# Kernel optimization log

Hardware: AMD Instinct MI355X
Metric: run time of the kernel (lower is better)

Reference implementation:

```python
import jax, jax.numpy as jnp
import numpy as np

B, T, V, E, H, S, C, VF, A, L = 32, 32, 32000, 512, 512, 512, 256, 512, 256, 50


def setup_inputs() -> dict:
    key = jax.random.key(0)
    ks = jax.random.split(key, 17)
    sc = lambda k, shp, fan: (jax.random.normal(k, shp, jnp.float32) / np.sqrt(fan)).astype(jnp.float32)
    inp = {
        "tgt": jax.random.randint(ks[0], (B, T), 0, V, dtype=jnp.int64),
        "decoder_state": jax.random.normal(ks[1], (B, H), jnp.float32),
        "category": jax.random.normal(ks[2], (B, C), jnp.float32),
        "v_feature": jax.random.normal(ks[3], (B, VF), jnp.float32),
        "session_outputs": jax.random.normal(ks[4], (B, L, S), jnp.float32),
        "session_mask": jnp.ones((B, L), dtype=bool),
        # learned parameters
        "emb": sc(ks[5], (V, E), E),
        "attn_Wh": sc(ks[6], (H, A), H),
        "attn_Ws": sc(ks[7], (S, A), S),
        "attn_b": jnp.zeros((A,), jnp.float32),
        "attn_v": sc(ks[8], (A,), A),
        "W_ih": sc(ks[9], (3 * H, E + S + C + VF), H),
        "W_hh": sc(ks[10], (3 * H, H), H),
        "b_ih": jnp.zeros((3 * H,), jnp.float32),
        "b_hh": jnp.zeros((3 * H,), jnp.float32),
        "W_out": 0.1 * jax.random.normal(ks[11], (V, H), jnp.float32),  # init.normal_(0, 0.1)
        "b_out": jnp.zeros((V,), jnp.float32),
    }
    return inp


def reference(tgt, decoder_state, category, v_feature, session_outputs, session_mask,
              emb, attn_Wh, attn_Ws, attn_b, attn_v, W_ih, W_hh, b_ih, b_hh, W_out, b_out):
    neg = jnp.finfo(session_outputs.dtype).min
    x = jnp.swapaxes(emb[tgt], 0, 1)                       # T,B,E
    sess_proj = jnp.einsum('bls,sa->bla', session_outputs, attn_Ws) + attn_b  # precompute key proj

    def step(h, x_t):
        # additive (Bahdanau) session attention on last-layer state h: B,H
        q = (h @ attn_Wh)[:, None, :]                      # B,1,A
        e = jnp.einsum('bla,a->bl', jnp.tanh(q + sess_proj), attn_v)
        e = jnp.where(session_mask, e, neg)
        a = jax.nn.softmax(e, axis=-1)                     # B,L
        ctx = jnp.einsum('bl,blh->bh', a, session_outputs)
        inp = jnp.concatenate([x_t, ctx, category, v_feature], axis=-1)
        # single-step GRU (PyTorch gate order: reset, update, new)
        gx = inp @ W_ih.T + b_ih
        gh = h @ W_hh.T + b_hh
        xr, xz, xn = jnp.split(gx, 3, axis=-1)
        hr, hz, hn = jnp.split(gh, 3, axis=-1)
        r = jax.nn.sigmoid(xr + hr)
        z = jax.nn.sigmoid(xz + hz)
        n = jnp.tanh(xn + r * hn)
        h2 = (1.0 - z) * n + z * h
        vocab = h2 @ W_out.T + b_out
        return h2, (vocab, h2)

    _, (vocab_outputs, outputs) = jax.lax.scan(step, decoder_state, x)
    return jnp.swapaxes(vocab_outputs, 0, 1), jnp.swapaxes(outputs, 0, 1)
```

## Files before the change

kernel.cpp:

```cpp
#include <hip/hip_runtime.h>

typedef unsigned short u16;
typedef unsigned int u32;
typedef __attribute__((ext_vector_type(8))) short short8;
typedef __attribute__((ext_vector_type(4))) float f32x4;

#define NB 32
#define NT 32
#define NV 32000
#define NE 512
#define NH 512
#define NS 512
#define NC 256
#define NVF 512
#define NA 256
#define NL 50
#define G3 1536
#define NWB 1792

__device__ __forceinline__ float bf2f(u16 u) {
  union { u32 i; float f; } v; v.i = ((u32)u) << 16; return v.f;
}
__device__ __forceinline__ u16 f2bf(float f) {
  union { float f; u32 i; } v; v.f = f;
  u32 x = v.i;
  return (u16)((x + 0x7fffu + ((x >> 16) & 1u)) >> 16);
}
__device__ __forceinline__ float sigmoidf_(float x) { return 1.f / (1.f + __expf(-x)); }
__device__ __forceinline__ float tanhf_(float x) {
  x = fminf(fmaxf(x, -15.f), 15.f);
  float e = __expf(2.f * x);
  return (e - 1.f) / (e + 1.f);
}
__device__ __forceinline__ void cvt8(u16* dst, const float* src) {
  f32x4 a = *(const f32x4*)src;
  f32x4 b = *(const f32x4*)(src + 4);
  short8 o;
  o[0] = (short)f2bf(a[0]); o[1] = (short)f2bf(a[1]);
  o[2] = (short)f2bf(a[2]); o[3] = (short)f2bf(a[3]);
  o[4] = (short)f2bf(b[0]); o[5] = (short)f2bf(b[1]);
  o[6] = (short)f2bf(b[2]); o[7] = (short)f2bf(b[3]);
  *(short8*)dst = o;
}

__global__ __launch_bounds__(256) void prep_kernel(
    const int* __restrict__ tgt, const float* __restrict__ dec,
    const float* __restrict__ cat, const float* __restrict__ vfe,
    const float* __restrict__ sess, const float* __restrict__ emb,
    const float* __restrict__ Wh, const float* __restrict__ Ws,
    const float* __restrict__ Wih, const float* __restrict__ Whh,
    const float* __restrict__ Wout,
    u16* __restrict__ WB, u16* __restrict__ Wx, u16* __restrict__ Wc,
    u16* __restrict__ X, u16* __restrict__ Ah, float* __restrict__ h_ws,
    u16* __restrict__ Wob, u16* __restrict__ Wst, u16* __restrict__ sessb,
    u16* __restrict__ cvb, u16* __restrict__ Wcv)
{
  int blk = blockIdx.x, tid = threadIdx.x;
  if (blk < 448) {
    int base = (blk * 256 + tid) * 8, j = base >> 9, c = base & 511;
    if (j < G3) cvt8(WB + base, Whh + (size_t)j * 512 + c);
    else {
      int a = j - G3;
      short8 o;
      #pragma unroll
      for (int i = 0; i < 8; i++) o[i] = (short)f2bf(Wh[(size_t)(c + i) * NA + a]);
      *(short8*)(WB + base) = o;
    }
  } else if (blk < 832) {
    int base = ((blk - 448) * 256 + tid) * 8, j = base >> 9, c = base & 511;
    cvt8(Wx + base, Wih + (size_t)j * 1792 + c);
  } else if (blk < 1216) {
    int base = ((blk - 832) * 256 + tid) * 8, j = base >> 9, c = base & 511;
    cvt8(Wc + base, Wih + (size_t)j * 1792 + 512 + c);
  } else if (blk < 1472) {
    int base = ((blk - 1216) * 256 + tid) * 8, tb = base >> 9, e = base & 511;
    cvt8(X + base, emb + (size_t)tgt[tb] * NE + e);
  } else if (blk < 1480) {
    int base = ((blk - 1472) * 256 + tid) * 8;
    cvt8(Ah + base, dec + base);
  } else if (blk < 1488) {
    int base = ((blk - 1480) * 256 + tid) * 8;
    *(f32x4*)(h_ws + base) = *(const f32x4*)(dec + base);
    *(f32x4*)(h_ws + base + 4) = *(const f32x4*)(dec + base + 4);
  } else if (blk < 9488) {
    int base = ((blk - 1488) * 256 + tid) * 8;
    cvt8(Wob + base, Wout + base);
  } else if (blk < 9552) {
    int base = ((blk - 9488) * 256 + tid) * 8, a = base >> 9, s = base & 511;
    short8 o;
    #pragma unroll
    for (int i = 0; i < 8; i++) o[i] = (short)f2bf(Ws[(size_t)(s + i) * NA + a]);
    *(short8*)(Wst + base) = o;
  } else if (blk < 9952) {
    int base = ((blk - 9552) * 256 + tid) * 8;
    cvt8(sessb + base, sess + base);
  } else if (blk < 9964) {
    int base = ((blk - 9952) * 256 + tid) * 8, b = base / 768, c = base % 768;
    if (c < NC) cvt8(cvb + base, cat + (size_t)b * NC + c);
    else        cvt8(cvb + base, vfe + (size_t)b * NVF + (c - NC));
  } else {
    int base = ((blk - 9964) * 256 + tid) * 8, j = base / 768, c = base % 768;
    cvt8(Wcv + base, Wih + (size_t)j * 1792 + 1024 + c);
  }
}

__global__ __launch_bounds__(256) void att_step2(
    int t,
    const float* __restrict__ sp, const float* __restrict__ av,
    const u16* __restrict__ SP2, const float* __restrict__ g2,
    const float* __restrict__ gx, const float* __restrict__ gstat,
    const float* __restrict__ bhh,
    float* __restrict__ h_ws, u16* __restrict__ Ah,
    float* __restrict__ h_out, u16* __restrict__ h_bf)
{
  int b = blockIdx.x, tid = threadIdx.x;
  __shared__ float q_s[256];
  __shared__ float e_s[64];
  __shared__ float a_s[64];
  __shared__ float gc_s[G3];

  q_s[tid] = g2[(size_t)b * NWB + G3 + tid];
  __syncthreads();

  if (tid < 200) {
    int l2 = tid >> 2, grp = tid & 3;
    const float* spr = sp + ((size_t)b * NL + l2) * NA + grp * 64;
    const float* avp = av + grp * 64;
    float part = 0.f;
    #pragma unroll 8
    for (int j = 0; j < 64; j++)
      part += tanhf_(q_s[grp * 64 + j] + spr[j]) * avp[j];
    part += __shfl_xor(part, 1);
    part += __shfl_xor(part, 2);
    if (grp == 0) e_s[l2] = part;
  }
  __syncthreads();
  if (tid < 64) {
    float x = (tid < NL) ? e_s[tid] : -3.0e38f;
    float m = x;
    #pragma unroll
    for (int o = 1; o < 64; o <<= 1) m = fmaxf(m, __shfl_xor(m, o));
    float p = (tid < NL) ? __expf(x - m) : 0.f;
    float ssum = p;
    #pragma unroll
    for (int o = 1; o < 64; o <<= 1) ssum += __shfl_xor(ssum, o);
    a_s[tid] = p / ssum;
  }
  __syncthreads();

  {
    const u16* sp2b = SP2 + (size_t)b * NL * G3;
    #pragma unroll
    for (int s = 0; s < 6; s++) {
      int j = s * 256 + tid;
      float acc = 0.f;
      #pragma unroll 5
      for (int l = 0; l < NL; l++)
        acc += a_s[l] * bf2f(sp2b[(size_t)l * G3 + j]);
      gc_s[j] = acc;
    }
  }
  __syncthreads();

  const float* gxr = gx + ((size_t)b * NT + t) * G3;
  const float* gsr = gstat + (size_t)b * G3;
  const float* ghr = g2 + (size_t)b * NWB;
  #pragma unroll
  for (int s = 0; s < 2; s++) {
    int k = tid + s * 256;
    float hprev = h_ws[b * NH + k];
    float rr = sigmoidf_(gxr[k] + gsr[k] + ghr[k] + gc_s[k] + bhh[k]);
    float zz = sigmoidf_(gxr[512 + k] + gsr[512 + k] + ghr[512 + k] + gc_s[512 + k] + bhh[512 + k]);
    float hn = ghr[1024 + k] + bhh[1024 + k];
    float xn = gxr[1024 + k] + gsr[1024 + k] + gc_s[1024 + k];
    float nn = tanhf_(xn + rr * hn);
    float h2 = (1.f - zz) * nn + zz * hprev;
    u16 hb = f2bf(h2);
    h_ws[b * NH + k] = h2;
    Ah[b * NH + k] = hb;
    h_out[((size_t)b * NT + t) * NH + k] = h2;
    h_bf[((size_t)b * NT + t) * NH + k] = hb;
  }
}

template<int BM, bool BIAS, typename OutT>
__global__ __launch_bounds__(256) void gemm_bt(
    const u16* __restrict__ Aw, int lda, const u16* __restrict__ Bw, int ldb,
    OutT* __restrict__ Cw, int ldc, const float* __restrict__ bias, int K, int nblk)
{
  int bn = blockIdx.x % nblk, bm = blockIdx.x / nblk;
  int w = threadIdx.x >> 6, l = threadIdx.x & 63;
  int lr = l & 15, kb = (l >> 4) * 8, r0 = (l >> 4) * 4;
  int n0 = bn * 64 + w * 16;
  constexpr int MT = BM / 16;
  f32x4 acc[MT];
  #pragma unroll
  for (int i = 0; i < MT; i++) acc[i] = (f32x4){0.f, 0.f, 0.f, 0.f};
  const u16* bp = Bw + (size_t)(n0 + lr) * ldb + kb;
  const u16* ap = Aw + (size_t)(bm * BM + lr) * lda + kb;
  #pragma unroll 4
  for (int k0 = 0; k0 < K; k0 += 32) {
    short8 bfr = *(const short8*)(bp + k0);
    #pragma unroll
    for (int mt = 0; mt < MT; mt++) {
      short8 afr = *(const short8*)(ap + (size_t)mt * 16 * lda + k0);
      acc[mt] = __builtin_amdgcn_mfma_f32_16x16x32_bf16(afr, bfr, acc[mt], 0, 0, 0);
    }
  }
  int col = n0 + lr;
  float bv = 0.f;
  if constexpr (BIAS) bv = bias[col];
  #pragma unroll
  for (int mt = 0; mt < MT; mt++) {
    #pragma unroll
    for (int i = 0; i < 4; i++) {
      int row = bm * BM + mt * 16 + r0 + i;
      float v = acc[mt][i] + bv;
      if constexpr (sizeof(OutT) == 2) Cw[(size_t)row * ldc + col] = f2bf(v);
      else                             Cw[(size_t)row * ldc + col] = v;
    }
  }
}

__global__ __launch_bounds__(256) void vocab_gemm(
    const u16* __restrict__ Aw, const u16* __restrict__ Bw,
    const float* __restrict__ bias, float* __restrict__ Cw)
{
  int bn = blockIdx.x % 500, bm = blockIdx.x / 500;
  int tid = threadIdx.x;
  int w = tid >> 6, l = tid & 63;
  int lr = l & 15, kb = (l >> 4) * 8, r0 = (l >> 4) * 4;
  int n0 = bn * 64;
  int m0 = bm * 256 + w * 64;
  f32x4 acc[4][4];
  #pragma unroll
  for (int i = 0; i < 4; i++)
    #pragma unroll
    for (int j = 0; j < 4; j++) acc[i][j] = (f32x4){0.f, 0.f, 0.f, 0.f};
  const u16* ap = Aw + (size_t)(m0 + lr) * 512 + kb;
  const u16* bp = Bw + (size_t)(n0 + lr) * 512 + kb;
  #pragma unroll 2
  for (int k0 = 0; k0 < 512; k0 += 32) {
    short8 bfr[4], afr[4];
    #pragma unroll
    for (int nt = 0; nt < 4; nt++) bfr[nt] = *(const short8*)(bp + (size_t)nt * 16 * 512 + k0);
    #pragma unroll
    for (int mt = 0; mt < 4; mt++) afr[mt] = *(const short8*)(ap + (size_t)mt * 16 * 512 + k0);
    #pragma unroll
    for (int mt = 0; mt < 4; mt++)
      #pragma unroll
      for (int nt = 0; nt < 4; nt++)
        acc[mt][nt] = __builtin_amdgcn_mfma_f32_16x16x32_bf16(afr[mt], bfr[nt], acc[mt][nt], 0, 0, 0);
  }
  __shared__ float cs[64 * 68];
  int crow = tid >> 4, ccol = (tid & 15) * 4;
  f32x4 bb = *(const f32x4*)(bias + n0 + ccol);
  #pragma unroll
  for (int g = 0; g < 4; g++) {
    __syncthreads();
    #pragma unroll
    for (int nt = 0; nt < 4; nt++)
      #pragma unroll
      for (int i = 0; i < 4; i++)
        cs[(w * 16 + r0 + i) * 68 + nt * 16 + lr] = acc[g][nt][i];
    __syncthreads();
    #pragma unroll
    for (int i = 0; i < 4; i++) {
      int s = crow * 4 + i;
      int ww = s >> 4;
      int grow = bm * 256 + ww * 64 + g * 16 + (s & 15);
      f32x4 v = *(f32x4*)(cs + s * 68 + ccol);
      v[0] += bb[0]; v[1] += bb[1]; v[2] += bb[2]; v[3] += bb[3];
      *(f32x4*)(Cw + (size_t)grow * NV + n0 + ccol) = v;
    }
  }
}

extern "C" void kernel_launch(void* const* d_in, const int* in_sizes, int n_in,
                              void* d_out, int out_size, void* d_ws, size_t ws_size,
                              hipStream_t stream)
{
  const int* tgt = (const int*)d_in[0];
  const float* dec = (const float*)d_in[1];
  const float* cat = (const float*)d_in[2];
  const float* vfe = (const float*)d_in[3];
  const float* sess = (const float*)d_in[4];
  const float* emb = (const float*)d_in[6];
  const float* Wh = (const float*)d_in[7];
  const float* Ws = (const float*)d_in[8];
  const float* ab = (const float*)d_in[9];
  const float* av = (const float*)d_in[10];
  const float* Wih = (const float*)d_in[11];
  const float* Whh = (const float*)d_in[12];
  const float* bih = (const float*)d_in[13];
  const float* bhh = (const float*)d_in[14];
  const float* Wout = (const float*)d_in[15];
  const float* bout = (const float*)d_in[16];

  float* out_vocab = (float*)d_out;
  float* h_out = out_vocab + (size_t)NB * NT * NV;

  float* sp = (float*)d_ws;
  float* gstat = sp + NB * NL * NA;
  float* gx = gstat + NB * G3;
  float* g2 = gx + (size_t)NB * NT * G3;
  float* h_ws = g2 + NB * NWB;
  u16* WB = (u16*)(h_ws + NB * NH);
  u16* Wx = WB + (size_t)NWB * 512;
  u16* Wc = Wx + (size_t)G3 * 512;
  u16* X = Wc + (size_t)G3 * 512;
  u16* Ah = X + (size_t)NB * NT * NE;
  u16* SP2 = Ah + NB * NH;
  u16* Wob = SP2 + (size_t)NB * NL * G3;
  u16* Wst = Wob + (size_t)NV * NH;
  u16* sessb = Wst + (size_t)NA * NS;
  u16* cvb = sessb + (size_t)NB * NL * NS;
  u16* Wcv = cvb + NB * 768;
  u16* h_bf = Wcv + (size_t)G3 * 768;

  prep_kernel<<<10540, 256, 0, stream>>>(tgt, dec, cat, vfe, sess, emb, Wh, Ws, Wih, Whh, Wout,
                                         WB, Wx, Wc, X, Ah, h_ws, Wob, Wst, sessb, cvb, Wcv);
  gemm_bt<64, false, float><<<16 * 24, 256, 0, stream>>>(X, 512, Wx, 512, gx, G3, nullptr, 512, 24);
  gemm_bt<64, true, float><<<25 * 4, 256, 0, stream>>>(sessb, 512, Wst, 512, sp, NA, ab, 512, 4);
  gemm_bt<32, true, float><<<24, 256, 0, stream>>>(cvb, 768, Wcv, 768, gstat, G3, bih, 768, 24);
  gemm_bt<64, false, u16><<<25 * 24, 256, 0, stream>>>(sessb, 512, Wc, 512, SP2, G3, nullptr, 512, 24);

  for (int t = 0; t < NT; t++) {
    gemm_bt<32, false, float><<<28, 256, 0, stream>>>(Ah, 512, WB, 512, g2, NWB, nullptr, 512, 28);
    att_step2<<<NB, 256, 0, stream>>>(t, sp, av, SP2, g2, gx, gstat, bhh, h_ws, Ah, h_out, h_bf);
  }
  vocab_gemm<<<4 * 500, 256, 0, stream>>>(h_bf, Wob, bout, out_vocab);
}
```

Measured before the change: 1.265 ms.

## Fuse recurrent step loop into one cooperative persistent kernel; restage vocab GEMM A in LDS

Replaces the 64 per-timestep launches (small h·WB GEMM plus attention/GRU kernel) with one cooperative kernel of 88 blocks. 56 blocks compute the recurrent GEMM and 32 blocks do attention and the GRU update, and the two groups hand off through grid-wide syncs. Per-batch session projections, biases and static gates are kept in shared memory, and h stays in shared memory between steps. The vocab GEMM is also restructured so the 256-row A tile is staged through LDS and each wave covers 16 columns across 16 M-tiles. The cost is grid.sync latency on every step and a large shared-memory footprint in the cooperative kernel.

```diff
diff --git a/kernel.cpp b/kernel.cpp
--- a/kernel.cpp
+++ b/kernel.cpp
@@ -1,4 +1,7 @@
 #include <hip/hip_runtime.h>
+#include <hip/hip_cooperative_groups.h>
+
+namespace cg = cooperative_groups;
 
 typedef unsigned short u16;
 typedef unsigned int u32;
@@ -51,7 +54,7 @@
     const float* __restrict__ Wih, const float* __restrict__ Whh,
     const float* __restrict__ Wout,
     u16* __restrict__ WB, u16* __restrict__ Wx, u16* __restrict__ Wc,
-    u16* __restrict__ X, u16* __restrict__ Ah, float* __restrict__ h_ws,
+    u16* __restrict__ X, u16* __restrict__ Ah,
     u16* __restrict__ Wob, u16* __restrict__ Wst, u16* __restrict__ sessb,
     u16* __restrict__ cvb, u16* __restrict__ Wcv)
 {
@@ -78,108 +81,152 @@
   } else if (blk < 1480) {
     int base = ((blk - 1472) * 256 + tid) * 8;
     cvt8(Ah + base, dec + base);
-  } else if (blk < 1488) {
+  } else if (blk < 9480) {
     int base = ((blk - 1480) * 256 + tid) * 8;
-    *(f32x4*)(h_ws + base) = *(const f32x4*)(dec + base);
-    *(f32x4*)(h_ws + base + 4) = *(const f32x4*)(dec + base + 4);
-  } else if (blk < 9488) {
-    int base = ((blk - 1488) * 256 + tid) * 8;
     cvt8(Wob + base, Wout + base);
-  } else if (blk < 9552) {
-    int base = ((blk - 9488) * 256 + tid) * 8, a = base >> 9, s = base & 511;
+  } else if (blk < 9544) {
+    int base = ((blk - 9480) * 256 + tid) * 8, a = base >> 9, s = base & 511;
     short8 o;
     #pragma unroll
     for (int i = 0; i < 8; i++) o[i] = (short)f2bf(Ws[(size_t)(s + i) * NA + a]);
     *(short8*)(Wst + base) = o;
-  } else if (blk < 9952) {
-    int base = ((blk - 9552) * 256 + tid) * 8;
+  } else if (blk < 9944) {
+    int base = ((blk - 9544) * 256 + tid) * 8;
     cvt8(sessb + base, sess + base);
-  } else if (blk < 9964) {
-    int base = ((blk - 9952) * 256 + tid) * 8, b = base / 768, c = base % 768;
+  } else if (blk < 9956) {
+    int base = ((blk - 9944) * 256 + tid) * 8, b = base / 768, c = base % 768;
     if (c < NC) cvt8(cvb + base, cat + (size_t)b * NC + c);
     else        cvt8(cvb + base, vfe + (size_t)b * NVF + (c - NC));
   } else {
-    int base = ((blk - 9964) * 256 + tid) * 8, j = base / 768, c = base % 768;
+    int base = ((blk - 9956) * 256 + tid) * 8, j = base / 768, c = base % 768;
     cvt8(Wcv + base, Wih + (size_t)j * 1792 + 1024 + c);
   }
 }
 
-__global__ __launch_bounds__(256) void att_step2(
-    int t,
+__global__ __launch_bounds__(256) void step_loop(
+    const u16* __restrict__ WB, const float* __restrict__ dec,
     const float* __restrict__ sp, const float* __restrict__ av,
-    const u16* __restrict__ SP2, const float* __restrict__ g2,
-    const float* __restrict__ gx, const float* __restrict__ gstat,
-    const float* __restrict__ bhh,
-    float* __restrict__ h_ws, u16* __restrict__ Ah,
+    const u16* __restrict__ SP2, const float* __restrict__ gx,
+    const float* __restrict__ gstat, const float* __restrict__ bhh,
+    float* __restrict__ g2, u16* __restrict__ Ah,
     float* __restrict__ h_out, u16* __restrict__ h_bf)
 {
-  int b = blockIdx.x, tid = threadIdx.x;
-  __shared__ float q_s[256];
-  __shared__ float e_s[64];
-  __shared__ float a_s[64];
-  __shared__ float gc_s[G3];
-
-  q_s[tid] = g2[(size_t)b * NWB + G3 + tid];
-  __syncthreads();
-
-  if (tid < 200) {
-    int l2 = tid >> 2, grp = tid & 3;
-    const float* spr = sp + ((size_t)b * NL + l2) * NA + grp * 64;
-    const float* avp = av + grp * 64;
-    float part = 0.f;
-    #pragma unroll 8
-    for (int j = 0; j < 64; j++)
-      part += tanhf_(q_s[grp * 64 + j] + spr[j]) * avp[j];
-    part += __shfl_xor(part, 1);
-    part += __shfl_xor(part, 2);
-    if (grp == 0) e_s[l2] = part;
-  }
-  __syncthreads();
-  if (tid < 64) {
-    float x = (tid < NL) ? e_s[tid] : -3.0e38f;
-    float m = x;
-    #pragma unroll
-    for (int o = 1; o < 64; o <<= 1) m = fmaxf(m, __shfl_xor(m, o));
-    float p = (tid < NL) ? __expf(x - m) : 0.f;
-    float ssum = p;
-    #pragma unroll
-    for (int o = 1; o < 64; o <<= 1) ssum += __shfl_xor(ssum, o);
-    a_s[tid] = p / ssum;
-  }
-  __syncthreads();
-
-  {
-    const u16* sp2b = SP2 + (size_t)b * NL * G3;
-    #pragma unroll
-    for (int s = 0; s < 6; s++) {
-      int j = s * 256 + tid;
-      float acc = 0.f;
-      #pragma unroll 5
-      for (int l = 0; l < NL; l++)
-        acc += a_s[l] * bf2f(sp2b[(size_t)l * G3 + j]);
-      gc_s[j] = acc;
-    }
-  }
-  __syncthreads();
-
-  const float* gxr = gx + ((size_t)b * NT + t) * G3;
-  const float* gsr = gstat + (size_t)b * G3;
-  const float* ghr = g2 + (size_t)b * NWB;
-  #pragma unroll
-  for (int s = 0; s < 2; s++) {
-    int k = tid + s * 256;
-    float hprev = h_ws[b * NH + k];
-    float rr = sigmoidf_(gxr[k] + gsr[k] + ghr[k] + gc_s[k] + bhh[k]);
-    float zz = sigmoidf_(gxr[512 + k] + gsr[512 + k] + ghr[512 + k] + gc_s[512 + k] + bhh[512 + k]);
-    float hn = ghr[1024 + k] + bhh[1024 + k];
-    float xn = gxr[1024 + k] + gsr[1024 + k] + gc_s[1024 + k];
-    float nn = tanhf_(xn + rr * hn);
-    float h2 = (1.f - zz) * nn + zz * hprev;
-    u16 hb = f2bf(h2);
-    h_ws[b * NH + k] = h2;
-    Ah[b * NH + k] = hb;
-    h_out[((size_t)b * NT + t) * NH + k] = h2;
-    h_bf[((size_t)b * NT + t) * NH + k] = hb;
+  cg::grid_group grid = cg::this_grid();
+  int bid = blockIdx.x, tid = threadIdx.x;
+
+  if (bid < 56) {
+    int n0 = bid * 32;
+    int w = tid >> 6, l = tid & 63;
+    int mt = w & 1, nt = w >> 1;
+    int lr = l & 15, kb = (l >> 4) * 8, r0 = (l >> 4) * 4;
+    const u16* bp = WB + (size_t)(n0 + nt * 16 + lr) * 512 + kb;
+    const u16* ap = Ah + (size_t)(mt * 16 + lr) * 512 + kb;
+    int col = n0 + nt * 16 + lr;
+    for (int t = 0; t < NT; t++) {
+      f32x4 acc = (f32x4){0.f, 0.f, 0.f, 0.f};
+      #pragma unroll 8
+      for (int k0 = 0; k0 < 512; k0 += 32) {
+        short8 afr = *(const short8*)(ap + k0);
+        short8 bfr = *(const short8*)(bp + k0);
+        acc = __builtin_amdgcn_mfma_f32_16x16x32_bf16(afr, bfr, acc, 0, 0, 0);
+      }
+      #pragma unroll
+      for (int i = 0; i < 4; i++)
+        g2[(size_t)(mt * 16 + r0 + i) * NWB + col] = acc[i];
+      __threadfence();
+      grid.sync();
+      grid.sync();
+    }
+  } else {
+    int b = bid - 56;
+    __shared__ float sp_s[NL * NA];
+    __shared__ float h_prev[512];
+    __shared__ float av_s[256];
+    __shared__ float bhh_s[G3];
+    __shared__ float gst_s[G3];
+    __shared__ float q_s[256];
+    __shared__ float e_s[64];
+    __shared__ float a_s[64];
+    __shared__ float gc_s[G3];
+
+    for (int i = tid; i < NL * NA; i += 256) sp_s[i] = sp[(size_t)b * NL * NA + i];
+    h_prev[tid] = dec[b * NH + tid];
+    h_prev[256 + tid] = dec[b * NH + 256 + tid];
+    av_s[tid] = av[tid];
+    #pragma unroll
+    for (int i = 0; i < 6; i++) {
+      int j = i * 256 + tid;
+      bhh_s[j] = bhh[j];
+      gst_s[j] = gstat[(size_t)b * G3 + j];
+    }
+
+    for (int t = 0; t < NT; t++) {
+      grid.sync();
+      q_s[tid] = g2[(size_t)b * NWB + G3 + tid];
+      __syncthreads();
+
+      if (tid < 200) {
+        int l2 = tid >> 2, grp = tid & 3;
+        const float* spr = sp_s + l2 * NA + grp * 64;
+        const float* avp = av_s + grp * 64;
+        float part = 0.f;
+        #pragma unroll 8
+        for (int j = 0; j < 64; j++)
+          part += tanhf_(q_s[grp * 64 + j] + spr[j]) * avp[j];
+        part += __shfl_xor(part, 1);
+        part += __shfl_xor(part, 2);
+        if (grp == 0) e_s[l2] = part;
+      }
+      __syncthreads();
+      if (tid < 64) {
+        float x = (tid < NL) ? e_s[tid] : -3.0e38f;
+        float m = x;
+        #pragma unroll
+        for (int o = 1; o < 64; o <<= 1) m = fmaxf(m, __shfl_xor(m, o));
+        float p = (tid < NL) ? __expf(x - m) : 0.f;
+        float ssum = p;
+        #pragma unroll
+        for (int o = 1; o < 64; o <<= 1) ssum += __shfl_xor(ssum, o);
+        a_s[tid] = p / ssum;
+      }
+      __syncthreads();
+
+      if (tid < 192) {
+        const u16* p = SP2 + (size_t)b * NL * G3 + tid * 8;
+        float acc[8] = {0.f,0.f,0.f,0.f,0.f,0.f,0.f,0.f};
+        #pragma unroll 5
+        for (int l = 0; l < NL; l++) {
+          short8 v = *(const short8*)(p + (size_t)l * G3);
+          float al = a_s[l];
+          #pragma unroll
+          for (int j = 0; j < 8; j++) acc[j] += al * bf2f((u16)v[j]);
+        }
+        #pragma unroll
+        for (int j = 0; j < 8; j++) gc_s[tid * 8 + j] = acc[j];
+      }
+      __syncthreads();
+
+      const float* gxr = gx + ((size_t)b * NT + t) * G3;
+      const float* ghr = g2 + (size_t)b * NWB;
+      #pragma unroll
+      for (int s = 0; s < 2; s++) {
+        int k = tid + s * 256;
+        float hprev = h_prev[k];
+        float rr = sigmoidf_(gxr[k] + gst_s[k] + ghr[k] + gc_s[k] + bhh_s[k]);
+        float zz = sigmoidf_(gxr[512 + k] + gst_s[512 + k] + ghr[512 + k] + gc_s[512 + k] + bhh_s[512 + k]);
+        float hn = ghr[1024 + k] + bhh_s[1024 + k];
+        float xn = gxr[1024 + k] + gst_s[1024 + k] + gc_s[1024 + k];
+        float nn = tanhf_(xn + rr * hn);
+        float h2 = (1.f - zz) * nn + zz * hprev;
+        u16 hb = f2bf(h2);
+        h_prev[k] = h2;
+        Ah[b * NH + k] = hb;
+        h_out[((size_t)b * NT + t) * NH + k] = h2;
+        h_bf[((size_t)b * NT + t) * NH + k] = hb;
+      }
+      __threadfence();
+      grid.sync();
+    }
   }
 }
 
@@ -226,52 +273,53 @@
     const u16* __restrict__ Aw, const u16* __restrict__ Bw,
     const float* __restrict__ bias, float* __restrict__ Cw)
 {
-  int bn = blockIdx.x % 500, bm = blockIdx.x / 500;
+  int bm = blockIdx.x / 500, bn = blockIdx.x % 500;
   int tid = threadIdx.x;
   int w = tid >> 6, l = tid & 63;
   int lr = l & 15, kb = (l >> 4) * 8, r0 = (l >> 4) * 4;
   int n0 = bn * 64;
-  int m0 = bm * 256 + w * 64;
-  f32x4 acc[4][4];
+  __shared__ __align__(16) u16 As[256 * 72];
+  f32x4 acc[16];
   #pragma unroll
-  for (int i = 0; i < 4; i++)
-    #pragma unroll
-    for (int j = 0; j < 4; j++) acc[i][j] = (f32x4){0.f, 0.f, 0.f, 0.f};
-  const u16* ap = Aw + (size_t)(m0 + lr) * 512 + kb;
-  const u16* bp = Bw + (size_t)(n0 + lr) * 512 + kb;
-  #pragma unroll 2
-  for (int k0 = 0; k0 < 512; k0 += 32) {
-    short8 bfr[4], afr[4];
-    #pragma unroll
-    for (int nt = 0; nt < 4; nt++) bfr[nt] = *(const short8*)(bp + (size_t)nt * 16 * 512 + k0);
-    #pragma unroll
-    for (int mt = 0; mt < 4; mt++) afr[mt] = *(const short8*)(ap + (size_t)mt * 16 * 512 + k0);
-    #pragma unroll
-    for (int mt = 0; mt < 4; mt++)
-      #pragma unroll
-      for (int nt = 0; nt < 4; nt++)
-        acc[mt][nt] = __builtin_amdgcn_mfma_f32_16x16x32_bf16(afr[mt], bfr[nt], acc[mt][nt], 0, 0, 0);
-  }
-  __shared__ float cs[64 * 68];
-  int crow = tid >> 4, ccol = (tid & 15) * 4;
-  f32x4 bb = *(const f32x4*)(bias + n0 + ccol);
+  for (int i = 0; i < 16; i++) acc[i] = (f32x4){0.f, 0.f, 0.f, 0.f};
+  const u16* bp = Bw + (size_t)(n0 + w * 16 + lr) * 512 + kb;
+  for (int ko = 0; ko < 512; ko += 64) {
+    __syncthreads();
+    #pragma unroll
+    for (int it = 0; it < 8; it++) {
+      int idx = it * 256 + tid;
+      int row = idx >> 3, c8 = (idx & 7) * 8;
+      *(short8*)(As + row * 72 + c8) = *(const short8*)(Aw + (size_t)(bm * 256 + row) * 512 + ko + c8);
+    }
+    __syncthreads();
+    #pragma unroll
+    for (int kc = 0; kc < 64; kc += 32) {
+      short8 bfr = *(const short8*)(bp + ko + kc);
+      #pragma unroll
+      for (int mt = 0; mt < 16; mt++) {
+        short8 afr = *(const short8*)(As + (mt * 16 + lr) * 72 + kc + kb);
+        acc[mt] = __builtin_amdgcn_mfma_f32_16x16x32_bf16(afr, bfr, acc[mt], 0, 0, 0);
+      }
+    }
+  }
+  float* cs = (float*)As;
+  int rr0 = tid >> 4, cc = (tid & 15) * 4;
+  f32x4 bb = *(const f32x4*)(bias + n0 + cc);
   #pragma unroll
   for (int g = 0; g < 4; g++) {
     __syncthreads();
     #pragma unroll
-    for (int nt = 0; nt < 4; nt++)
+    for (int m2 = 0; m2 < 4; m2++)
       #pragma unroll
       for (int i = 0; i < 4; i++)
-        cs[(w * 16 + r0 + i) * 68 + nt * 16 + lr] = acc[g][nt][i];
+        cs[(m2 * 16 + r0 + i) * 68 + w * 16 + lr] = acc[g * 4 + m2][i];
     __syncthreads();
     #pragma unroll
     for (int i = 0; i < 4; i++) {
-      int s = crow * 4 + i;
-      int ww = s >> 4;
-      int grow = bm * 256 + ww * 64 + g * 16 + (s & 15);
-      f32x4 v = *(f32x4*)(cs + s * 68 + ccol);
+      int rrow = rr0 + i * 16;
+      f32x4 v = *(f32x4*)(cs + rrow * 68 + cc);
       v[0] += bb[0]; v[1] += bb[1]; v[2] += bb[2]; v[3] += bb[3];
-      *(f32x4*)(Cw + (size_t)grow * NV + n0 + ccol) = v;
+      *(f32x4*)(Cw + (size_t)(bm * 256 + g * 64 + rrow) * NV + n0 + cc) = v;
     }
   }
 }
@@ -304,8 +352,7 @@
   float* gstat = sp + NB * NL * NA;
   float* gx = gstat + NB * G3;
   float* g2 = gx + (size_t)NB * NT * G3;
-  float* h_ws = g2 + NB * NWB;
-  u16* WB = (u16*)(h_ws + NB * NH);
+  u16* WB = (u16*)(g2 + NB * NWB);
   u16* Wx = WB + (size_t)NWB * 512;
   u16* Wc = Wx + (size_t)G3 * 512;
   u16* X = Wc + (size_t)G3 * 512;
@@ -318,16 +365,19 @@
   u16* Wcv = cvb + NB * 768;
   u16* h_bf = Wcv + (size_t)G3 * 768;
 
-  prep_kernel<<<10540, 256, 0, stream>>>(tgt, dec, cat, vfe, sess, emb, Wh, Ws, Wih, Whh, Wout,
-                                         WB, Wx, Wc, X, Ah, h_ws, Wob, Wst, sessb, cvb, Wcv);
+  prep_kernel<<<10532, 256, 0, stream>>>(tgt, dec, cat, vfe, sess, emb, Wh, Ws, Wih, Whh, Wout,
+                                         WB, Wx, Wc, X, Ah, Wob, Wst, sessb, cvb, Wcv);
   gemm_bt<64, false, float><<<16 * 24, 256, 0, stream>>>(X, 512, Wx, 512, gx, G3, nullptr, 512, 24);
   gemm_bt<64, true, float><<<25 * 4, 256, 0, stream>>>(sessb, 512, Wst, 512, sp, NA, ab, 512, 4);
   gemm_bt<32, true, float><<<24, 256, 0, stream>>>(cvb, 768, Wcv, 768, gstat, G3, bih, 768, 24);
   gemm_bt<64, false, u16><<<25 * 24, 256, 0, stream>>>(sessb, 512, Wc, 512, SP2, G3, nullptr, 512, 24);
 
-  for (int t = 0; t < NT; t++) {
-    gemm_bt<32, false, float><<<28, 256, 0, stream>>>(Ah, 512, WB, 512, g2, NWB, nullptr, 512, 28);
-    att_step2<<<NB, 256, 0, stream>>>(t, sp, av, SP2, g2, gx, gstat, bhh, h_ws, Ah, h_out, h_bf);
-  }
+  {
+    void* args[] = { (void*)&WB, (void*)&dec, (void*)&sp, (void*)&av, (void*)&SP2,
+                     (void*)&gx, (void*)&gstat, (void*)&bhh, (void*)&g2,
+                     (void*)&Ah, (void*)&h_out, (void*)&h_bf };
+    hipLaunchCooperativeKernel((const void*)step_loop, dim3(88), dim3(256), args, 0, stream);
+  }
+
   vocab_gemm<<<4 * 500, 256, 0, stream>>>(h_bf, Wob, bout, out_vocab);
 }
```

Result: slower. 1.711 ms (+35.2%).
